# Performance work log

Measured on AMD Instinct MI355X. Metric: run time of the kernel, lower is better.

## Reference

```python
import jax, jax.numpy as jnp
import numpy as np

B, L, V = 64, 512, 32000
E, H, D = 64, 512, 1024   # embed dim, LSTM hidden, bidirectional dim
NH, KD = 8, 64            # attention heads, key_dim
TOPK = 5
BN_EPS = 1e-3             # keras BatchNormalization default epsilon


def _run_lstm(x, Wx, Wh, b):
    """Keras-style LSTM (gate order i,f,g,o). x: [B,T,Din]. Returns (seq [B,T,H], last [B,H])."""
    Bn, Hn = x.shape[0], Wh.shape[0]
    z = jnp.einsum('btd,dk->btk', x, Wx) + b  # precompute input contribution [B,T,4H]
    def step(carry, zt):
        h, c = carry
        g = zt + h @ Wh
        i, f, gg, o = jnp.split(g, 4, axis=-1)
        c = jax.nn.sigmoid(f) * c + jax.nn.sigmoid(i) * jnp.tanh(gg)
        h = jax.nn.sigmoid(o) * jnp.tanh(c)
        return (h, c), h
    init = (jnp.zeros((Bn, Hn), x.dtype), jnp.zeros((Bn, Hn), x.dtype))
    (hT, _), hs = jax.lax.scan(step, init, jnp.swapaxes(z, 0, 1))
    return jnp.swapaxes(hs, 0, 1), hT


def _bilstm_seq(x, fWx, fWh, fb, bWx, bWh, bb):
    hf, _ = _run_lstm(x, fWx, fWh, fb)
    hb, _ = _run_lstm(x[:, ::-1], bWx, bWh, bb)
    return jnp.concatenate([hf, hb[:, ::-1]], axis=-1)


def _bilstm_last(x, fWx, fWh, fb, bWx, bWh, bb):
    _, hf = _run_lstm(x, fWx, fWh, fb)
    _, hb = _run_lstm(x[:, ::-1], bWx, bWh, bb)
    return jnp.concatenate([hf, hb], axis=-1)


def _cos(x):
    return x / (jnp.linalg.norm(x, axis=-1, keepdims=True) + 1e-6)


def _topk_gather(q, keys, values, k, weight=None):
    """Cosine-similarity top-k retrieval: q [B,64], keys/values [N,64] -> [B,k,64]."""
    sim = _cos(q) @ _cos(keys).T          # [B,N]
    if weight is not None:
        sim = sim * weight                # importance / confidence weighting
    _, idx = jax.lax.top_k(sim, k)
    return values[idx]                    # gather -> [B,k,64]


def _forward(tokens, emb,
             l1f_Wx, l1f_Wh, l1f_b, l1b_Wx, l1b_Wh, l1b_b,
             l2f_Wx, l2f_Wh, l2f_b, l2b_Wx, l2b_Wh, l2b_b,
             Wq, bq, Wk, bk, Wv, bv, Wo, bo,
             mq_W, mq_b,
             ext_keys, ext_vals, form_emb, conc_keys, conc_vals,
             st_mem, lt_mem, lt_imp, inf_mem, inf_conf,
             rs_W, rs_b, bn_gamma, bn_beta, bn_mean, bn_var,
             out_W, out_b, fin_W, fin_b):
    # _process_input
    x = emb[tokens]                                                   # [B,L,64]
    x = _bilstm_seq(x, l1f_Wx, l1f_Wh, l1f_b, l1b_Wx, l1b_Wh, l1b_b)  # [B,L,1024]
    x = _bilstm_last(x, l2f_Wx, l2f_Wh, l2f_b, l2b_Wx, l2b_Wh, l2b_b) # [B,1024]
    # _apply_attention: MHA over a length-1 sequence
    xs = x[:, None, :]                                                # [B,1,1024]
    q = jnp.einsum('bse,ehd->bshd', xs, Wq) + bq
    k = jnp.einsum('bse,ehd->bshd', xs, Wk) + bk
    v = jnp.einsum('bse,ehd->bshd', xs, Wv) + bv
    att = jax.nn.softmax(jnp.einsum('bshd,bthd->bhst', q, k) / jnp.sqrt(jnp.float32(KD)), axis=-1)
    ctx = jnp.einsum('bhst,bthd->bshd', att, v)
    x = (jnp.einsum('bshd,hde->bse', ctx, Wo) + bo)[:, 0]             # [B,1024]
    # _query_memories: six-bank gather/combine
    query = x @ mq_W + mq_b                                           # [B,64]
    m_ext = jax.nn.softmax(query @ ext_keys.T, axis=-1) @ ext_vals    # [B,64]
    m_form = _topk_gather(query, form_emb, form_emb, TOPK)            # [B,5,64]
    m_conc = _topk_gather(query, conc_keys, conc_vals, TOPK)          # [B,5,64]
    m_st = _topk_gather(query, st_mem, st_mem, TOPK)                  # [B,5,64]
    m_lt = _topk_gather(query, lt_mem, lt_mem, TOPK, weight=lt_imp)   # [B,5,64]
    m_inf = _topk_gather(query, inf_mem, inf_mem, TOPK, weight=inf_conf)
    mem = jnp.concatenate([m_ext[:, None], m_form, m_conc, m_st, m_lt, m_inf], axis=1)  # [B,26,64]
    x = jnp.mean(mem, axis=1)                                         # [B,64]
    # _apply_reasoning (training=False -> inference batchnorm)
    x = jax.nn.relu(x @ rs_W + rs_b)                                  # [B,512]
    x = (x - bn_mean) / jnp.sqrt(bn_var + BN_EPS) * bn_gamma + bn_beta
    # _generate_output (stage 'elementary1')
    x = x @ out_W + out_b                                             # [B,128]
    return jax.nn.sigmoid(x @ fin_W + fin_b)                          # [B,1]


def setup_inputs() -> dict:
    key = jax.random.key(0)
    ks = iter(jax.random.split(key, 64))
    def rn(shape, s=0.02):
        return jax.random.normal(next(ks), shape, dtype=jnp.float32) * s
    def z(shape):
        return jnp.zeros(shape, dtype=jnp.float32)
    inp = {
        'tokens': jax.random.randint(next(ks), (B, L), 0, V),
        'emb': rn((V, E), 0.05),
        'l1f_Wx': rn((E, 4 * H)), 'l1f_Wh': rn((H, 4 * H)), 'l1f_b': z((4 * H,)),
        'l1b_Wx': rn((E, 4 * H)), 'l1b_Wh': rn((H, 4 * H)), 'l1b_b': z((4 * H,)),
        'l2f_Wx': rn((D, 4 * H)), 'l2f_Wh': rn((H, 4 * H)), 'l2f_b': z((4 * H,)),
        'l2b_Wx': rn((D, 4 * H)), 'l2b_Wh': rn((H, 4 * H)), 'l2b_b': z((4 * H,)),
        'Wq': rn((D, NH, KD)), 'bq': z((NH, KD)),
        'Wk': rn((D, NH, KD)), 'bk': z((NH, KD)),
        'Wv': rn((D, NH, KD)), 'bv': z((NH, KD)),
        'Wo': rn((NH, KD, D)), 'bo': z((D,)),
        'mq_W': rn((D, 64)), 'mq_b': z((64,)),
        'ext_keys': rn((100, 64), 0.5), 'ext_vals': rn((100, 64), 0.5),
        'form_emb': rn((1000, 64), 0.5),
        'conc_keys': rn((1000, 64), 0.5), 'conc_vals': rn((1000, 64), 0.5),
        'st_mem': rn((100, 64), 0.5),
        'lt_mem': rn((10000, 64), 0.5),
        'lt_imp': jax.random.uniform(next(ks), (10000,), dtype=jnp.float32),
        'inf_mem': rn((500, 64), 0.5),
        'inf_conf': jax.random.uniform(next(ks), (500,), dtype=jnp.float32),
        'rs_W': rn((64, 512)), 'rs_b': z((512,)),
        'bn_gamma': jnp.ones((512,), jnp.float32), 'bn_beta': z((512,)),
        'bn_mean': rn((512,), 0.1), 'bn_var': jnp.ones((512,), jnp.float32),
        'out_W': rn((512, 128)), 'out_b': z((128,)),
        'fin_W': rn((128, 1)), 'fin_b': z((1,)),
    }
    return inp


def reference(tokens, emb,
              l1f_Wx, l1f_Wh, l1f_b, l1b_Wx, l1b_Wh, l1b_b,
              l2f_Wx, l2f_Wh, l2f_b, l2b_Wx, l2b_Wh, l2b_b,
              Wq, bq, Wk, bk, Wv, bv, Wo, bo,
              mq_W, mq_b,
              ext_keys, ext_vals, form_emb, conc_keys, conc_vals,
              st_mem, lt_mem, lt_imp, inf_mem, inf_conf,
              rs_W, rs_b, bn_gamma, bn_beta, bn_mean, bn_var,
              out_W, out_b, fin_W, fin_b):
    return _forward(tokens, emb,
                    l1f_Wx, l1f_Wh, l1f_b, l1b_Wx, l1b_Wh, l1b_b,
                    l2f_Wx, l2f_Wh, l2f_b, l2b_Wx, l2b_Wh, l2b_b,
                    Wq, bq, Wk, bk, Wv, bv, Wo, bo,
                    mq_W, mq_b,
                    ext_keys, ext_vals, form_emb, conc_keys, conc_vals,
                    st_mem, lt_mem, lt_imp, inf_mem, inf_conf,
                    rs_W, rs_b, bn_gamma, bn_beta, bn_mean, bn_var,
                    out_W, out_b, fin_W, fin_b)
```

## Files before the change

### kernel.cpp

```cpp
#include <hip/hip_runtime.h>
#include <cstddef>
#include <cstdint>

typedef short s8v   __attribute__((ext_vector_type(8)));
typedef float f32x4 __attribute__((ext_vector_type(4)));

__device__ __forceinline__ float b2f(unsigned short u) {
  union { unsigned u; float f; } x; x.u = ((unsigned)u) << 16; return x.f;
}
__device__ __forceinline__ unsigned short f2b(float f) {
  union { float f; unsigned u; } x; x.f = f;
  unsigned u = x.u;
  return (unsigned short)((u + 0x7FFFu + ((u >> 16) & 1u)) >> 16);
}
__device__ __forceinline__ float sigm(float x) { return 1.f / (1.f + __expf(-x)); }
__device__ __forceinline__ float tanh_(float x) { return 1.f - 2.f / (__expf(2.f * x) + 1.f); }

#define AT_LOAD(p)     __hip_atomic_load((p), __ATOMIC_RELAXED, __HIP_MEMORY_SCOPE_AGENT)
#define AT_STORE_RLX(p,v) __hip_atomic_store((p), (v), __ATOMIC_RELAXED, __HIP_MEMORY_SCOPE_AGENT)

__device__ __forceinline__ s8v ldg_b128_sc(const unsigned short* p) {
  s8v r;
  asm volatile("global_load_dwordx4 %0, %1, off sc0 sc1" : "=v"(r) : "v"(p) : "memory");
  return r;
}
__device__ __forceinline__ void stg_b128_sc(unsigned short* p, s8v v) {
  asm volatile("global_store_dwordx4 %0, %1, off sc0 sc1" :: "v"(p), "v"(v) : "memory");
}

__global__ void __launch_bounds__(256)
k_embed(const int* __restrict__ tok, const float* __restrict__ emb,
        unsigned short* __restrict__ x1)
{
  const int g = blockIdx.x * 256 + threadIdx.x;
  if (g >= 64 * 512 * 8) return;
  const int row = g >> 3, i = g & 7;
  const int t = tok[row];
  const f32x4 v0 = *(const f32x4*)(emb + (size_t)t * 64 + i * 8);
  const f32x4 v1 = *(const f32x4*)(emb + (size_t)t * 64 + i * 8 + 4);
  s8v o;
#pragma unroll
  for (int e = 0; e < 4; ++e) { o[e] = (short)f2b(v0[e]); o[4 + e] = (short)f2b(v1[e]); }
  *(s8v*)(x1 + (size_t)row * 64 + i * 8) = o;
}

__global__ void __launch_bounds__(256)
k_wxt(const float* __restrict__ Wf, const float* __restrict__ Wb,
      unsigned short* __restrict__ out)
{
  __shared__ float t[64][65];
  const int tid = threadIdx.x;
  const int kt = blockIdx.x, nt = blockIdx.y, dir = blockIdx.z;
  const float* W = dir ? Wb : Wf;
#pragma unroll
  for (int i = 0; i < 16; ++i) {
    const int c = i * 256 + tid;
    const int k = c >> 6, n = c & 63;
    t[k][n] = W[(size_t)(kt * 64 + k) * 2048 + nt * 64 + n];
  }
  __syncthreads();
#pragma unroll
  for (int i = 0; i < 16; ++i) {
    const int c = i * 256 + tid;
    const int n = c >> 6, k = c & 63;
    out[(size_t)dir * 2048 * 1024 + (size_t)(nt * 64 + n) * 1024 + kt * 64 + k] = f2b(t[k][n]);
  }
}

__global__ void __launch_bounds__(256)
k_norms(const float* __restrict__ formE, const float* __restrict__ concK,
        const float* __restrict__ stM, const float* __restrict__ ltM,
        const float* __restrict__ infM, float* __restrict__ inn)
{
  const int i = blockIdx.x * 256 + threadIdx.x;
  if (i >= 12600) return;
  const float* src; int loc;
  if (i < 1000)       { src = formE; loc = i; }
  else if (i < 2000)  { src = concK; loc = i - 1000; }
  else if (i < 2100)  { src = stM;   loc = i - 2000; }
  else if (i < 12100) { src = ltM;   loc = i - 2100; }
  else                { src = infM;  loc = i - 12100; }
  float ss = 0.f;
#pragma unroll 16
  for (int d = 0; d < 64; ++d) { const float v = src[(size_t)loc * 64 + d]; ss += v * v; }
  inn[i] = 1.f / (sqrtf(ss) + 1e-6f);
}

template<int PHASE>
__global__ void __launch_bounds__(128, 1)
k_lstm(const unsigned short* __restrict__ xin,
       const unsigned short* __restrict__ z2fp, const unsigned short* __restrict__ z2bp,
       const float* __restrict__ Whf, const float* __restrict__ Whb,
       const float* __restrict__ Wxf, const float* __restrict__ Wxb,
       const float* __restrict__ bsf, const float* __restrict__ bsb,
       unsigned short* __restrict__ hbuf,
       unsigned short* __restrict__ yout,
       int* __restrict__ flags,
       float* __restrict__ cg,
       int s0, int s1, int CT)
{
  __shared__ unsigned short h_lds[64 * 512];
  __shared__ unsigned short x_lds[64 * 64];
  __shared__ float g_lds[2][64 * 64];
  __shared__ float c_lds[64 * 16];
  __shared__ float bias_lds[64];

  const int tid  = threadIdx.x;
  const int wv   = tid >> 6;
  const int lane = tid & 63;
  const int wg   = blockIdx.x & 31;
  const int dir  = blockIdx.x >> 5;
  const int j0   = wg * 16;
  const int fc   = lane & 15;
  const int fk   = (lane >> 4) << 3;

  const float* Wh = dir ? Whb : Whf;
  const float* Wx = dir ? Wxb : Wxf;
  const unsigned short* Z2 = dir ? z2bp : z2fp;
  const float* BS = dir ? bsb : bsf;
  int* flg = flags + dir * 32;
  unsigned short* hb = hbuf + (size_t)dir * (2 * 64 * 512);

  for (int i = tid; i < 64; i += 128) bias_lds[i] = BS[(i >> 4) * 512 + j0 + (i & 15)];
  if (PHASE == 1 || s0 == 0) {
    for (int i = tid; i < 1024; i += 128) c_lds[i] = 0.f;
  } else {
    for (int i = tid; i < 1024; i += 128)
      c_lds[i] = cg[(size_t)dir * 64 * 512 + (i >> 4) * 512 + j0 + (i & 15)];
  }

  s8v Bh[4][8];
#pragma unroll
  for (int nt = 0; nt < 4; ++nt) {
    const int col = nt * 512 + j0 + fc;
#pragma unroll
    for (int kk = 0; kk < 8; ++kk) {
      const int kb = wv * 256 + kk * 32 + fk;
      s8v f;
#pragma unroll
      for (int i = 0; i < 8; ++i) f[i] = (short)f2b(Wh[(size_t)(kb + i) * 2048 + col]);
      Bh[nt][kk] = f;
    }
  }
  s8v Bx[4];
  if (PHASE == 1) {
#pragma unroll
    for (int nt = 0; nt < 4; ++nt) {
      const int col = nt * 512 + j0 + fc;
      const int kb = wv * 32 + fk;
      s8v f;
#pragma unroll
      for (int i = 0; i < 8; ++i) f[i] = (short)f2b(Wx[(size_t)(kb + i) * 2048 + col]);
      Bx[nt] = f;
    }
  }
  __syncthreads();

  for (int s = s0; s < s1; ++s) {
    const int t = dir ? (511 - s) : s;

    s8v zreg[4];
    if (PHASE == 1) {
#pragma unroll
      for (int i = 0; i < 4; ++i) {
        const int c = i * 128 + tid;
        const int row = c >> 3, kb = c & 7;
        s8v v = *(const s8v*)(xin + ((size_t)row * 512 + t) * 64 + kb * 8);
        *(s8v*)((char*)x_lds + row * 128 + ((kb * 16) ^ ((row & 7) << 4))) = v;
      }
    } else {
      const int gb = tid >> 1, jh = tid & 1;
      const int lt = dir ? (s1 - 1 - s) : (s - s0);
#pragma unroll
      for (int g = 0; g < 4; ++g)
        zreg[g] = *(const s8v*)(Z2 + ((size_t)(gb * CT + lt)) * 2048 + g * 512 + j0 + jh * 8);
    }

    if (s > 0) {
      const int target = s;
      int spins = 0;
      for (;;) {
        int v = (lane < 32) ? AT_LOAD(&flg[lane]) : target;
        if (__all(v >= target)) break;
        if (++spins > (1 << 18)) break;
        __builtin_amdgcn_s_sleep(1);
      }
      const unsigned short* hsrc = hb + (size_t)((s - 1) & 1) * (64 * 512);
      s8v tmp[16];
#pragma unroll
      for (int r = 0; r < 2; ++r) {
#pragma unroll
        for (int i = 0; i < 16; ++i) {
          const int c = (r * 16 + i) * 128 + tid;
          const int row = c >> 6, kb = c & 63;
          tmp[i] = ldg_b128_sc(hsrc + (size_t)row * 512 + kb * 8);
        }
        asm volatile("s_waitcnt vmcnt(0)" ::: "memory");
        __builtin_amdgcn_sched_barrier(0);
#pragma unroll
        for (int i = 0; i < 16; ++i) {
          const int c = (r * 16 + i) * 128 + tid;
          const int row = c >> 6, kb = c & 63;
          *(s8v*)((char*)h_lds + row * 1024 + ((kb * 16) ^ ((row & 7) << 4))) = tmp[i];
        }
      }
    }
    __syncthreads();

    f32x4 acc[4][4];
#pragma unroll
    for (int mt = 0; mt < 4; ++mt)
#pragma unroll
      for (int nt = 0; nt < 4; ++nt) acc[mt][nt] = (f32x4){0.f, 0.f, 0.f, 0.f};

    if (PHASE == 1) {
      const int kx2 = (wv * 32 + fk) * 2;
#pragma unroll
      for (int mt = 0; mt < 4; ++mt) {
        const int row = mt * 16 + fc;
        s8v a = *(const s8v*)((char*)x_lds + row * 128 + (kx2 ^ ((row & 7) << 4)));
#pragma unroll
        for (int nt = 0; nt < 4; ++nt)
          acc[mt][nt] = __builtin_amdgcn_mfma_f32_16x16x32_bf16(a, Bx[nt], acc[mt][nt], 0, 0, 0);
      }
    }
    if (s > 0) {
#pragma unroll
      for (int kk = 0; kk < 8; ++kk) {
        const int k2 = (wv * 256 + kk * 32 + fk) * 2;
        s8v a[4];
#pragma unroll
        for (int mt = 0; mt < 4; ++mt) {
          const int row = mt * 16 + fc;
          a[mt] = *(const s8v*)((char*)h_lds + row * 1024 + (k2 ^ ((row & 7) << 4)));
        }
#pragma unroll
        for (int mt = 0; mt < 4; ++mt)
#pragma unroll
          for (int nt = 0; nt < 4; ++nt)
            acc[mt][nt] = __builtin_amdgcn_mfma_f32_16x16x32_bf16(a[mt], Bh[nt][kk], acc[mt][nt], 0, 0, 0);
      }
    }
    {
      const int r0 = (lane >> 4) << 2;
#pragma unroll
      for (int mt = 0; mt < 4; ++mt)
#pragma unroll
        for (int nt = 0; nt < 4; ++nt) {
          const int colj = nt * 16 + fc;
          const int row0 = mt * 16 + r0;
#pragma unroll
          for (int r = 0; r < 4; ++r)
            g_lds[wv][(row0 + r) * 64 + colj] = acc[mt][nt][r];
        }
    }
    __syncthreads();

    {
      const int gb = tid >> 1, jh = tid & 1;
      const float* g0 = g_lds[0] + gb * 64;
      const float* g1 = g_lds[1] + gb * 64;
      s8v hv;
#pragma unroll
      for (int jj = 0; jj < 8; ++jj) {
        const int j = jh * 8 + jj;
        float pi = g0[0 * 16 + j] + g1[0 * 16 + j] + bias_lds[0 * 16 + j];
        float pf = g0[1 * 16 + j] + g1[1 * 16 + j] + bias_lds[1 * 16 + j];
        float pg = g0[2 * 16 + j] + g1[2 * 16 + j] + bias_lds[2 * 16 + j];
        float po = g0[3 * 16 + j] + g1[3 * 16 + j] + bias_lds[3 * 16 + j];
        if (PHASE == 2) {
          pi += b2f((unsigned short)zreg[0][jj]);
          pf += b2f((unsigned short)zreg[1][jj]);
          pg += b2f((unsigned short)zreg[2][jj]);
          po += b2f((unsigned short)zreg[3][jj]);
        }
        const int ci = gb * 16 + j;
        const float c = sigm(pf) * c_lds[ci] + sigm(pi) * tanh_(pg);
        c_lds[ci] = c;
        hv[jj] = (short)f2b(sigm(po) * tanh_(c));
      }
      stg_b128_sc(hb + (size_t)(s & 1) * (64 * 512) + gb * 512 + j0 + jh * 8, hv);
      if (PHASE == 1) {
        *(s8v*)(yout + ((size_t)gb * 512 + t) * 1024 + dir * 512 + j0 + jh * 8) = hv;
      } else if (s == 511) {
        *(s8v*)(yout + (size_t)gb * 1024 + dir * 512 + j0 + jh * 8) = hv;
      }
    }
    if (PHASE == 2 && s == s1 - 1 && s1 < 512) {
      __syncthreads();
      for (int i = tid; i < 1024; i += 128)
        cg[(size_t)dir * 64 * 512 + (i >> 4) * 512 + j0 + (i & 15)] = c_lds[i];
    }
    __syncthreads();
    if (tid == 0) AT_STORE_RLX(&flg[wg], s + 1);
  }
}

__global__ void __launch_bounds__(256)
k_zgemm(const unsigned short* __restrict__ A, const unsigned short* __restrict__ Wxt,
        unsigned short* __restrict__ Cf, unsigned short* __restrict__ Cb,
        int tb0, int tb1, int CT)
{
  __shared__ unsigned short As[128 * 64];
  __shared__ unsigned short Bs[128 * 64];
  const int tid = threadIdx.x;
  const int lane = tid & 63;
  const int w = tid >> 6;
  const int wm = w >> 1, wn = w & 1;
  const int bx = blockIdx.x, by = blockIdx.y, dz = blockIdx.z;
  const unsigned short* Bmat = Wxt + (size_t)dz * 2048 * 1024;
  unsigned short* C = dz ? Cb : Cf;
  const int tb = dz ? tb1 : tb0;
  const int fc = lane & 15, fk = (lane >> 4) << 3;

  f32x4 acc[4][4];
#pragma unroll
  for (int mt = 0; mt < 4; ++mt)
#pragma unroll
    for (int nt = 0; nt < 4; ++nt) acc[mt][nt] = (f32x4){0.f, 0.f, 0.f, 0.f};

  for (int kt = 0; kt < 16; ++kt) {
    __syncthreads();
#pragma unroll
    for (int i = 0; i < 4; ++i) {
      const int c = i * 256 + tid;
      const int row = c >> 3, kb = c & 7;
      const int m = by * 128 + row;
      const int b = m / CT, lt = m - b * CT;
      s8v v = *(const s8v*)(A + ((size_t)b * 512 + tb + lt) * 1024 + kt * 64 + kb * 8);
      *(s8v*)((char*)As + row * 128 + ((kb * 16) ^ ((row & 7) << 4))) = v;
    }
#pragma unroll
    for (int i = 0; i < 4; ++i) {
      const int c = i * 256 + tid;
      const int n = c >> 3, kb = c & 7;
      s8v v = *(const s8v*)(Bmat + (size_t)(bx * 128 + n) * 1024 + kt * 64 + kb * 8);
      *(s8v*)((char*)Bs + n * 128 + ((kb * 16) ^ ((n & 7) << 4))) = v;
    }
    __syncthreads();
#pragma unroll
    for (int kk = 0; kk < 2; ++kk) {
      const int k2 = (kk * 32 + fk) * 2;
      s8v a[4], bfr[4];
#pragma unroll
      for (int mt = 0; mt < 4; ++mt) {
        const int row = wm * 64 + mt * 16 + fc;
        a[mt] = *(const s8v*)((char*)As + row * 128 + (k2 ^ ((row & 7) << 4)));
      }
#pragma unroll
      for (int nt = 0; nt < 4; ++nt) {
        const int n = wn * 64 + nt * 16 + fc;
        bfr[nt] = *(const s8v*)((char*)Bs + n * 128 + (k2 ^ ((n & 7) << 4)));
      }
#pragma unroll
      for (int mt = 0; mt < 4; ++mt)
#pragma unroll
        for (int nt = 0; nt < 4; ++nt)
          acc[mt][nt] = __builtin_amdgcn_mfma_f32_16x16x32_bf16(a[mt], bfr[nt], acc[mt][nt], 0, 0, 0);
    }
  }
  const int r0 = (lane >> 4) << 2;
#pragma unroll
  for (int mt = 0; mt < 4; ++mt)
#pragma unroll
    for (int nt = 0; nt < 4; ++nt) {
      const size_t rowg = (size_t)(by * 128 + wm * 64 + mt * 16 + r0);
      const int colg = bx * 128 + wn * 64 + nt * 16 + fc;
#pragma unroll
      for (int r = 0; r < 4; ++r)
        C[(rowg + r) * 2048 + colg] = f2b(acc[mt][nt][r]);
    }
}

__global__ void __launch_bounds__(256)
k_head1(const unsigned short* __restrict__ x2,
        const float* __restrict__ Wv, const float* __restrict__ bv,
        const float* __restrict__ Wo, const float* __restrict__ bo,
        const float* __restrict__ mqW, const float* __restrict__ mqb,
        float* __restrict__ query)
{
  __shared__ float xs[1024], ys[512], x3[1024];
  __shared__ float part[4][64];
  const int b = blockIdx.x, tid = threadIdx.x;
  for (int i = tid; i < 1024; i += 256) xs[i] = b2f(x2[(size_t)b * 1024 + i]);
  __syncthreads();
  {
    const int o = tid * 2;
    float a0 = 0.f, a1 = 0.f;
#pragma unroll 8
    for (int e = 0; e < 1024; ++e) {
      const float xv = xs[e];
      a0 += xv * Wv[(size_t)e * 512 + o];
      a1 += xv * Wv[(size_t)e * 512 + o + 1];
    }
    ys[o] = a0 + bv[o];
    ys[o + 1] = a1 + bv[o + 1];
  }
  __syncthreads();
  {
    const int e0 = tid * 4;
    float a0 = 0.f, a1 = 0.f, a2 = 0.f, a3 = 0.f;
#pragma unroll 8
    for (int h = 0; h < 512; ++h) {
      const float yv = ys[h];
      a0 += yv * Wo[(size_t)h * 1024 + e0];
      a1 += yv * Wo[(size_t)h * 1024 + e0 + 1];
      a2 += yv * Wo[(size_t)h * 1024 + e0 + 2];
      a3 += yv * Wo[(size_t)h * 1024 + e0 + 3];
    }
    x3[e0] = a0 + bo[e0];
    x3[e0 + 1] = a1 + bo[e0 + 1];
    x3[e0 + 2] = a2 + bo[e0 + 2];
    x3[e0 + 3] = a3 + bo[e0 + 3];
  }
  __syncthreads();
  {
    const int o = tid & 63, kc = tid >> 6;
    float a = 0.f;
#pragma unroll 8
    for (int e = kc * 256; e < kc * 256 + 256; ++e) a += x3[e] * mqW[(size_t)e * 64 + o];
    part[kc][o] = a;
  }
  __syncthreads();
  if (tid < 64)
    query[b * 64 + tid] = part[0][tid] + part[1][tid] + part[2][tid] + part[3][tid] + mqb[tid];
}

__device__ void bank_topk(const float* __restrict__ K, const float* __restrict__ V,
                          int n, const float* __restrict__ W, const float* __restrict__ inn,
                          float qinv, const float* q, float* sims, float* red, int* redi,
                          float* acc64, int tid)
{
  for (int i = tid; i < n; i += 256) {
    float s = 0.f;
#pragma unroll 16
    for (int d = 0; d < 64; ++d) s += q[d] * K[(size_t)i * 64 + d];
    s *= qinv * inn[i];
    if (W) s *= W[i];
    sims[i] = s;
  }
  __syncthreads();
  for (int it = 0; it < 5; ++it) {
    float bv = -1e30f; int bi = 1 << 30;
    for (int i = tid; i < n; i += 256) {
      const float v = sims[i];
      if (v > bv) { bv = v; bi = i; }
    }
    red[tid] = bv; redi[tid] = bi;
    __syncthreads();
    for (int st = 128; st >= 1; st >>= 1) {
      if (tid < st) {
        const float v = red[tid + st]; const int ix = redi[tid + st];
        if (v > red[tid] || (v == red[tid] && ix < redi[tid])) { red[tid] = v; redi[tid] = ix; }
      }
      __syncthreads();
    }
    const int sel = redi[0];
    if (tid < 64) acc64[tid] += V[(size_t)sel * 64 + tid];
    if (tid == 0) sims[sel] = -1e30f;
    __syncthreads();
  }
}

__global__ void __launch_bounds__(256)
k_head2(const float* __restrict__ query,
        const float* extK, const float* extV,
        const float* formE, const float* concK, const float* concV,
        const float* stM, const float* ltM, const float* ltW,
        const float* infM, const float* infW,
        const float* __restrict__ inn,
        const float* rsW, const float* rsb,
        const float* gma, const float* bta,
        const float* mea, const float* vr,
        const float* outW, const float* outb,
        const float* finW, const float* finb,
        float* __restrict__ out)
{
  __shared__ float q[64];
  __shared__ float acc64[64];
  __shared__ float sims[10000];
  __shared__ float red[256];
  __shared__ int redi[256];
  __shared__ float r1[512];
  __shared__ float o2[128];

  const int b = blockIdx.x, tid = threadIdx.x;
  if (tid < 64) q[tid] = query[b * 64 + tid];
  __syncthreads();
  red[tid] = (tid < 64) ? q[tid] * q[tid] : 0.f;
  __syncthreads();
  for (int st = 128; st >= 1; st >>= 1) { if (tid < st) red[tid] += red[tid + st]; __syncthreads(); }
  const float qinv = 1.f / (sqrtf(red[0]) + 1e-6f);
  __syncthreads();

  if (tid < 100) {
    float s = 0.f;
#pragma unroll 16
    for (int d = 0; d < 64; ++d) s += q[d] * extK[(size_t)tid * 64 + d];
    sims[tid] = s;
  }
  __syncthreads();
  red[tid] = (tid < 100) ? sims[tid] : -1e30f;
  __syncthreads();
  for (int st = 128; st >= 1; st >>= 1) { if (tid < st && red[tid + st] > red[tid]) red[tid] = red[tid + st]; __syncthreads(); }
  const float mx = red[0];
  __syncthreads();
  red[tid] = (tid < 100) ? __expf(sims[tid] - mx) : 0.f;
  __syncthreads();
  for (int st = 128; st >= 1; st >>= 1) { if (tid < st) red[tid] += red[tid + st]; __syncthreads(); }
  const float Z = red[0];
  __syncthreads();
  if (tid < 100) sims[tid] = __expf(sims[tid] - mx) / Z;
  __syncthreads();
  if (tid < 64) {
    float a = 0.f;
    for (int i = 0; i < 100; ++i) a += sims[i] * extV[(size_t)i * 64 + tid];
    acc64[tid] = a;
  }
  __syncthreads();

  bank_topk(formE, formE, 1000,  nullptr, inn + 0,     qinv, q, sims, red, redi, acc64, tid);
  bank_topk(concK, concV, 1000,  nullptr, inn + 1000,  qinv, q, sims, red, redi, acc64, tid);
  bank_topk(stM,   stM,   100,   nullptr, inn + 2000,  qinv, q, sims, red, redi, acc64, tid);
  bank_topk(ltM,   ltM,   10000, ltW,     inn + 2100,  qinv, q, sims, red, redi, acc64, tid);
  bank_topk(infM,  infM,  500,   infW,    inn + 12100, qinv, q, sims, red, redi, acc64, tid);

  if (tid < 64) acc64[tid] *= (1.f / 26.f);
  __syncthreads();

  {
    const int o = tid * 2;
    float a0 = 0.f, a1 = 0.f;
#pragma unroll 16
    for (int d = 0; d < 64; ++d) {
      const float xv = acc64[d];
      a0 += xv * rsW[(size_t)d * 512 + o];
      a1 += xv * rsW[(size_t)d * 512 + o + 1];
    }
    a0 = fmaxf(a0 + rsb[o], 0.f);
    a1 = fmaxf(a1 + rsb[o + 1], 0.f);
    r1[o]     = (a0 - mea[o])     / sqrtf(vr[o]     + 1e-3f) * gma[o]     + bta[o];
    r1[o + 1] = (a1 - mea[o + 1]) / sqrtf(vr[o + 1] + 1e-3f) * gma[o + 1] + bta[o + 1];
  }
  __syncthreads();
  if (tid < 128) {
    float a = 0.f;
#pragma unroll 8
    for (int j = 0; j < 512; ++j) a += r1[j] * outW[(size_t)j * 128 + tid];
    o2[tid] = a + outb[tid];
  }
  __syncthreads();
  red[tid] = (tid < 128) ? o2[tid] * finW[tid] : 0.f;
  __syncthreads();
  for (int st = 128; st >= 1; st >>= 1) { if (tid < st) red[tid] += red[tid + st]; __syncthreads(); }
  if (tid == 0) out[b] = sigm(red[0] + finb[0]);
}

__global__ void k_diag(float* out, int n, float val) {
  const int i = blockIdx.x * 64 + threadIdx.x;
  if (i < n) out[i] = val;
}

extern "C" void kernel_launch(void* const* d_in, const int* in_sizes, int n_in,
                              void* d_out, int out_size, void* d_ws, size_t ws_size,
                              hipStream_t stream)
{
  (void)in_sizes; (void)n_in;
  const int*   tokens = (const int*)d_in[0];
  const float* emb    = (const float*)d_in[1];
  const float* l1fWx  = (const float*)d_in[2];
  const float* l1fWh  = (const float*)d_in[3];
  const float* l1fb   = (const float*)d_in[4];
  const float* l1bWx  = (const float*)d_in[5];
  const float* l1bWh  = (const float*)d_in[6];
  const float* l1bb   = (const float*)d_in[7];
  const float* l2fWx  = (const float*)d_in[8];
  const float* l2fWh  = (const float*)d_in[9];
  const float* l2fb   = (const float*)d_in[10];
  const float* l2bWx  = (const float*)d_in[11];
  const float* l2bWh  = (const float*)d_in[12];
  const float* l2bb   = (const float*)d_in[13];
  const float* Wv     = (const float*)d_in[18];
  const float* bv     = (const float*)d_in[19];
  const float* Wo     = (const float*)d_in[20];
  const float* bo     = (const float*)d_in[21];
  const float* mqW    = (const float*)d_in[22];
  const float* mqb    = (const float*)d_in[23];
  const float* extK   = (const float*)d_in[24];
  const float* extV   = (const float*)d_in[25];
  const float* formE  = (const float*)d_in[26];
  const float* concK  = (const float*)d_in[27];
  const float* concV  = (const float*)d_in[28];
  const float* stM    = (const float*)d_in[29];
  const float* ltM    = (const float*)d_in[30];
  const float* ltW    = (const float*)d_in[31];
  const float* infM   = (const float*)d_in[32];
  const float* infW   = (const float*)d_in[33];
  const float* rsW    = (const float*)d_in[34];
  const float* rsb    = (const float*)d_in[35];
  const float* gma    = (const float*)d_in[36];
  const float* bta    = (const float*)d_in[37];
  const float* mea    = (const float*)d_in[38];
  const float* vr     = (const float*)d_in[39];
  const float* outW   = (const float*)d_in[40];
  const float* outb   = (const float*)d_in[41];
  const float* finW   = (const float*)d_in[42];
  const float* finb   = (const float*)d_in[43];

  float* outp = (float*)d_out;
  char* ws = (char*)d_ws;

  size_t off = 0;
  auto take = [&](size_t sz) { size_t o = off; off += (sz + 255) & ~(size_t)255; return o; };
  const size_t o_x1    = take((size_t)64 * 512 * 64 * 2);
  const size_t o_y1    = take((size_t)64 * 512 * 1024 * 2);
  const size_t o_wxt   = take((size_t)2 * 2048 * 1024 * 2);
  const size_t o_h1    = take((size_t)2 * 2 * 64 * 512 * 2);
  const size_t o_h2    = take((size_t)2 * 2 * 64 * 512 * 2);
  const size_t o_cg    = take((size_t)2 * 64 * 512 * 4);
  const size_t o_x2    = take((size_t)64 * 1024 * 2);
  const size_t o_query = take((size_t)64 * 64 * 4);
  const size_t o_norms = take((size_t)12600 * 4);
  const size_t o_flags = take(512);
  const size_t base = off;

  int CT = 0;
  const int cts[6] = {512, 256, 128, 64, 32, 16};
  for (int i = 0; i < 6; ++i) {
    const size_t need = base + (size_t)cts[i] * 524288 + 256;
    if (need <= ws_size) { CT = cts[i]; break; }
  }
  if (CT == 0) {
    k_diag<<<1, 64, 0, stream>>>(outp, out_size, (float)(ws_size >> 20));
    return;
  }
  const size_t o_zc = take((size_t)CT * 524288);

  unsigned short* x1   = (unsigned short*)(ws + o_x1);
  unsigned short* y1   = (unsigned short*)(ws + o_y1);
  unsigned short* wxt  = (unsigned short*)(ws + o_wxt);
  unsigned short* h1   = (unsigned short*)(ws + o_h1);
  unsigned short* h2   = (unsigned short*)(ws + o_h2);
  float*          cg   = (float*)(ws + o_cg);
  unsigned short* x2   = (unsigned short*)(ws + o_x2);
  float*          qry  = (float*)(ws + o_query);
  float*          nrm  = (float*)(ws + o_norms);
  int*            flags = (int*)(ws + o_flags);
  unsigned short* zcf  = (unsigned short*)(ws + o_zc);
  unsigned short* zcb  = zcf + (size_t)64 * CT * 2048;

  hipMemsetAsync(flags, 0, 512, stream);
  k_embed<<<1024, 256, 0, stream>>>(tokens, emb, x1);
  k_norms<<<50, 256, 0, stream>>>(formE, concK, stM, ltM, infM, nrm);
  k_wxt<<<dim3(16, 32, 2), 256, 0, stream>>>(l2fWx, l2bWx, wxt);

  k_lstm<1><<<64, 128, 0, stream>>>(x1, nullptr, nullptr, l1fWh, l1bWh, l1fWx, l1bWx,
                                    l1fb, l1bb, h1, y1, flags, nullptr, 0, 512, 512);

  const int nC = 512 / CT;
  for (int c = 0; c < nC; ++c) {
    const int s0 = c * CT, s1 = s0 + CT;
    k_zgemm<<<dim3(16, (64 * CT) / 128, 2), 256, 0, stream>>>(
        y1, wxt, zcf, zcb, s0, 512 - s1, CT);
    k_lstm<2><<<64, 128, 0, stream>>>(nullptr, zcf, zcb, l2fWh, l2bWh, nullptr, nullptr,
                                      l2fb, l2bb, h2, x2, flags + 64, cg, s0, s1, CT);
  }

  k_head1<<<64, 256, 0, stream>>>(x2, Wv, bv, Wo, bo, mqW, mqb, qry);
  k_head2<<<64, 256, 0, stream>>>(qry, extK, extV, formE, concK, concV, stM, ltM, ltW,
                                  infM, infW, nrm, rsW, rsb, gma, bta, mea, vr,
                                  outW, outb, finW, finb, outp);
}
```

Baseline: 7.066 ms.

## Split LSTM recurrence by batch rows per wave, removing cross-wave K reduction

The recurrent step used to split the K dimension across the two waves and then reduce partial gates through LDS with an extra barrier. It now gives each wave 32 batch rows over the full K=512, so gate activations are computed straight from MFMA accumulators, and the cell state lives in registers. Recurrent weights are pre-transposed to bf16 by a generic transpose kernel so they load as vector reads. The h load is also split so the first half is written to LDS while the second half is still in flight. In exchange, each thread now holds twice as many weight registers (64 s8v), which raises register pressure and could cause spills.

```diff
diff --git a/kernel.cpp b/kernel.cpp
--- a/kernel.cpp
+++ b/kernel.cpp
@@ -16,7 +16,7 @@
 __device__ __forceinline__ float sigm(float x) { return 1.f / (1.f + __expf(-x)); }
 __device__ __forceinline__ float tanh_(float x) { return 1.f - 2.f / (__expf(2.f * x) + 1.f); }
 
-#define AT_LOAD(p)     __hip_atomic_load((p), __ATOMIC_RELAXED, __HIP_MEMORY_SCOPE_AGENT)
+#define AT_LOAD(p)        __hip_atomic_load((p), __ATOMIC_RELAXED, __HIP_MEMORY_SCOPE_AGENT)
 #define AT_STORE_RLX(p,v) __hip_atomic_store((p), (v), __ATOMIC_RELAXED, __HIP_MEMORY_SCOPE_AGENT)
 
 __device__ __forceinline__ s8v ldg_b128_sc(const unsigned short* p) {
@@ -45,8 +45,8 @@
 }
 
 __global__ void __launch_bounds__(256)
-k_wxt(const float* __restrict__ Wf, const float* __restrict__ Wb,
-      unsigned short* __restrict__ out)
+k_tr(const float* __restrict__ Wf, const float* __restrict__ Wb,
+     unsigned short* __restrict__ out, int K, int N)
 {
   __shared__ float t[64][65];
   const int tid = threadIdx.x;
@@ -56,14 +56,14 @@
   for (int i = 0; i < 16; ++i) {
     const int c = i * 256 + tid;
     const int k = c >> 6, n = c & 63;
-    t[k][n] = W[(size_t)(kt * 64 + k) * 2048 + nt * 64 + n];
+    t[k][n] = W[(size_t)(kt * 64 + k) * N + nt * 64 + n];
   }
   __syncthreads();
 #pragma unroll
   for (int i = 0; i < 16; ++i) {
     const int c = i * 256 + tid;
     const int n = c >> 6, k = c & 63;
-    out[(size_t)dir * 2048 * 1024 + (size_t)(nt * 64 + n) * 1024 + kt * 64 + k] = f2b(t[k][n]);
+    out[(size_t)dir * N * K + (size_t)(nt * 64 + n) * K + kt * 64 + k] = f2b(t[k][n]);
   }
 }
 
@@ -90,7 +90,7 @@
 __global__ void __launch_bounds__(128, 1)
 k_lstm(const unsigned short* __restrict__ xin,
        const unsigned short* __restrict__ z2fp, const unsigned short* __restrict__ z2bp,
-       const float* __restrict__ Whf, const float* __restrict__ Whb,
+       const unsigned short* __restrict__ wht,
        const float* __restrict__ Wxf, const float* __restrict__ Wxb,
        const float* __restrict__ bsf, const float* __restrict__ bsb,
        unsigned short* __restrict__ hbuf,
@@ -99,81 +99,81 @@
        float* __restrict__ cg,
        int s0, int s1, int CT)
 {
-  __shared__ unsigned short h_lds[64 * 512];
-  __shared__ unsigned short x_lds[64 * 64];
-  __shared__ float g_lds[2][64 * 64];
-  __shared__ float c_lds[64 * 16];
-  __shared__ float bias_lds[64];
+  __shared__ __align__(16) unsigned short h_lds[64 * 512];
+  __shared__ __align__(16) unsigned short z_lds[64 * 72];
+  __shared__ __align__(16) unsigned short hout[16 * 72];
 
   const int tid  = threadIdx.x;
-  const int wv   = tid >> 6;
+  const int w    = tid >> 6;
   const int lane = tid & 63;
+  const int fc   = lane & 15, fg = lane >> 4;
   const int wg   = blockIdx.x & 31;
   const int dir  = blockIdx.x >> 5;
   const int j0   = wg * 16;
-  const int fc   = lane & 15;
-  const int fk   = (lane >> 4) << 3;
-
-  const float* Wh = dir ? Whb : Whf;
+
+  const unsigned short* Wht = wht + (size_t)dir * 2048 * 512;
   const float* Wx = dir ? Wxb : Wxf;
   const unsigned short* Z2 = dir ? z2bp : z2fp;
   const float* BS = dir ? bsb : bsf;
   int* flg = flags + dir * 32;
   unsigned short* hb = hbuf + (size_t)dir * (2 * 64 * 512);
 
-  for (int i = tid; i < 64; i += 128) bias_lds[i] = BS[(i >> 4) * 512 + j0 + (i & 15)];
+  float bias_reg[4];
+#pragma unroll
+  for (int nt = 0; nt < 4; ++nt) bias_reg[nt] = BS[nt * 512 + j0 + fc];
+
+  float c_reg[8];
   if (PHASE == 1 || s0 == 0) {
-    for (int i = tid; i < 1024; i += 128) c_lds[i] = 0.f;
+#pragma unroll
+    for (int i = 0; i < 8; ++i) c_reg[i] = 0.f;
   } else {
-    for (int i = tid; i < 1024; i += 128)
-      c_lds[i] = cg[(size_t)dir * 64 * 512 + (i >> 4) * 512 + j0 + (i & 15)];
-  }
-
-  s8v Bh[4][8];
-#pragma unroll
-  for (int nt = 0; nt < 4; ++nt) {
-    const int col = nt * 512 + j0 + fc;
-#pragma unroll
-    for (int kk = 0; kk < 8; ++kk) {
-      const int kb = wv * 256 + kk * 32 + fk;
-      s8v f;
-#pragma unroll
-      for (int i = 0; i < 8; ++i) f[i] = (short)f2b(Wh[(size_t)(kb + i) * 2048 + col]);
-      Bh[nt][kk] = f;
-    }
-  }
-  s8v Bx[4];
+#pragma unroll
+    for (int mt = 0; mt < 2; ++mt)
+#pragma unroll
+      for (int v = 0; v < 4; ++v)
+        c_reg[mt * 4 + v] =
+          cg[(size_t)dir * 32768 + (size_t)(w * 32 + mt * 16 + fg * 4 + v) * 512 + j0 + fc];
+  }
+
+  s8v Bh[4][16];
+#pragma unroll
+  for (int nt = 0; nt < 4; ++nt)
+#pragma unroll
+    for (int kk = 0; kk < 16; ++kk)
+      Bh[nt][kk] = *(const s8v*)(Wht + (size_t)(nt * 512 + j0 + fc) * 512 + kk * 32 + fg * 8);
+
+  s8v Bx[4][2];
   if (PHASE == 1) {
 #pragma unroll
-    for (int nt = 0; nt < 4; ++nt) {
-      const int col = nt * 512 + j0 + fc;
-      const int kb = wv * 32 + fk;
-      s8v f;
-#pragma unroll
-      for (int i = 0; i < 8; ++i) f[i] = (short)f2b(Wx[(size_t)(kb + i) * 2048 + col]);
-      Bx[nt] = f;
-    }
-  }
-  __syncthreads();
+    for (int nt = 0; nt < 4; ++nt)
+#pragma unroll
+      for (int kx = 0; kx < 2; ++kx) {
+        s8v f;
+#pragma unroll
+        for (int i = 0; i < 8; ++i)
+          f[i] = (short)f2b(Wx[(size_t)(kx * 32 + fg * 8 + i) * 2048 + nt * 512 + j0 + fc]);
+        Bx[nt][kx] = f;
+      }
+  }
 
   for (int s = s0; s < s1; ++s) {
     const int t = dir ? (511 - s) : s;
-
-    s8v zreg[4];
+    const int gb = tid >> 1, jh = tid & 1;
+
+    s8v xf[2][2];
+    s8v zr[4];
     if (PHASE == 1) {
 #pragma unroll
-      for (int i = 0; i < 4; ++i) {
-        const int c = i * 128 + tid;
-        const int row = c >> 3, kb = c & 7;
-        s8v v = *(const s8v*)(xin + ((size_t)row * 512 + t) * 64 + kb * 8);
-        *(s8v*)((char*)x_lds + row * 128 + ((kb * 16) ^ ((row & 7) << 4))) = v;
-      }
+      for (int mt = 0; mt < 2; ++mt)
+#pragma unroll
+        for (int kx = 0; kx < 2; ++kx)
+          xf[mt][kx] = *(const s8v*)(xin +
+            ((size_t)(w * 32 + mt * 16 + fc) * 512 + t) * 64 + kx * 32 + fg * 8);
     } else {
-      const int gb = tid >> 1, jh = tid & 1;
       const int lt = dir ? (s1 - 1 - s) : (s - s0);
 #pragma unroll
       for (int g = 0; g < 4; ++g)
-        zreg[g] = *(const s8v*)(Z2 + ((size_t)(gb * CT + lt)) * 2048 + g * 512 + j0 + jh * 8);
+        zr[g] = *(const s8v*)(Z2 + ((size_t)(gb * CT + lt)) * 2048 + g * 512 + j0 + jh * 8);
     }
 
     if (s > 0) {
@@ -186,110 +186,114 @@
         __builtin_amdgcn_s_sleep(1);
       }
       const unsigned short* hsrc = hb + (size_t)((s - 1) & 1) * (64 * 512);
-      s8v tmp[16];
-#pragma unroll
-      for (int r = 0; r < 2; ++r) {
-#pragma unroll
-        for (int i = 0; i < 16; ++i) {
-          const int c = (r * 16 + i) * 128 + tid;
-          const int row = c >> 6, kb = c & 63;
-          tmp[i] = ldg_b128_sc(hsrc + (size_t)row * 512 + kb * 8);
-        }
-        asm volatile("s_waitcnt vmcnt(0)" ::: "memory");
-        __builtin_amdgcn_sched_barrier(0);
-#pragma unroll
-        for (int i = 0; i < 16; ++i) {
-          const int c = (r * 16 + i) * 128 + tid;
-          const int row = c >> 6, kb = c & 63;
-          *(s8v*)((char*)h_lds + row * 1024 + ((kb * 16) ^ ((row & 7) << 4))) = tmp[i];
-        }
-      }
+      s8v t0[16], t1[16];
+#pragma unroll
+      for (int i = 0; i < 16; ++i) {
+        const int c = i * 128 + tid;
+        t0[i] = ldg_b128_sc(hsrc + (size_t)(c >> 6) * 512 + (c & 63) * 8);
+      }
+#pragma unroll
+      for (int i = 0; i < 16; ++i) {
+        const int c = (16 + i) * 128 + tid;
+        t1[i] = ldg_b128_sc(hsrc + (size_t)(c >> 6) * 512 + (c & 63) * 8);
+      }
+      asm volatile("s_waitcnt vmcnt(16)" ::: "memory");
+      __builtin_amdgcn_sched_barrier(0);
+#pragma unroll
+      for (int i = 0; i < 16; ++i) {
+        const int c = i * 128 + tid;
+        const int row = c >> 6, kb = c & 63;
+        *(s8v*)((char*)h_lds + row * 1024 + ((kb * 16) ^ ((row & 7) << 4))) = t0[i];
+      }
+      asm volatile("s_waitcnt vmcnt(0)" ::: "memory");
+      __builtin_amdgcn_sched_barrier(0);
+#pragma unroll
+      for (int i = 0; i < 16; ++i) {
+        const int c = (16 + i) * 128 + tid;
+        const int row = c >> 6, kb = c & 63;
+        *(s8v*)((char*)h_lds + row * 1024 + ((kb * 16) ^ ((row & 7) << 4))) = t1[i];
+      }
+    }
+    if (PHASE == 2) {
+#pragma unroll
+      for (int g = 0; g < 4; ++g)
+        *(s8v*)(z_lds + gb * 72 + g * 16 + jh * 8) = zr[g];
     }
     __syncthreads();
 
-    f32x4 acc[4][4];
-#pragma unroll
-    for (int mt = 0; mt < 4; ++mt)
+    f32x4 acc[2][4];
+#pragma unroll
+    for (int mt = 0; mt < 2; ++mt)
 #pragma unroll
       for (int nt = 0; nt < 4; ++nt) acc[mt][nt] = (f32x4){0.f, 0.f, 0.f, 0.f};
 
     if (PHASE == 1) {
-      const int kx2 = (wv * 32 + fk) * 2;
-#pragma unroll
-      for (int mt = 0; mt < 4; ++mt) {
-        const int row = mt * 16 + fc;
-        s8v a = *(const s8v*)((char*)x_lds + row * 128 + (kx2 ^ ((row & 7) << 4)));
-#pragma unroll
-        for (int nt = 0; nt < 4; ++nt)
-          acc[mt][nt] = __builtin_amdgcn_mfma_f32_16x16x32_bf16(a, Bx[nt], acc[mt][nt], 0, 0, 0);
-      }
+#pragma unroll
+      for (int kx = 0; kx < 2; ++kx)
+#pragma unroll
+        for (int mt = 0; mt < 2; ++mt)
+#pragma unroll
+          for (int nt = 0; nt < 4; ++nt)
+            acc[mt][nt] = __builtin_amdgcn_mfma_f32_16x16x32_bf16(xf[mt][kx], Bx[nt][kx], acc[mt][nt], 0, 0, 0);
     }
     if (s > 0) {
 #pragma unroll
-      for (int kk = 0; kk < 8; ++kk) {
-        const int k2 = (wv * 256 + kk * 32 + fk) * 2;
-        s8v a[4];
-#pragma unroll
-        for (int mt = 0; mt < 4; ++mt) {
-          const int row = mt * 16 + fc;
+      for (int kk = 0; kk < 16; ++kk) {
+        const int k2 = (kk * 32 + fg * 8) * 2;
+        s8v a[2];
+#pragma unroll
+        for (int mt = 0; mt < 2; ++mt) {
+          const int row = w * 32 + mt * 16 + fc;
           a[mt] = *(const s8v*)((char*)h_lds + row * 1024 + (k2 ^ ((row & 7) << 4)));
         }
 #pragma unroll
-        for (int mt = 0; mt < 4; ++mt)
+        for (int mt = 0; mt < 2; ++mt)
 #pragma unroll
           for (int nt = 0; nt < 4; ++nt)
             acc[mt][nt] = __builtin_amdgcn_mfma_f32_16x16x32_bf16(a[mt], Bh[nt][kk], acc[mt][nt], 0, 0, 0);
       }
     }
+
+#pragma unroll
+    for (int mt = 0; mt < 2; ++mt)
+#pragma unroll
+      for (int v = 0; v < 4; ++v) {
+        const int b = w * 32 + mt * 16 + fg * 4 + v;
+        float pi = acc[mt][0][v] + bias_reg[0];
+        float pf = acc[mt][1][v] + bias_reg[1];
+        float pg = acc[mt][2][v] + bias_reg[2];
+        float po = acc[mt][3][v] + bias_reg[3];
+        if (PHASE == 2) {
+          pi += b2f(z_lds[b * 72 + 0 * 16 + fc]);
+          pf += b2f(z_lds[b * 72 + 1 * 16 + fc]);
+          pg += b2f(z_lds[b * 72 + 2 * 16 + fc]);
+          po += b2f(z_lds[b * 72 + 3 * 16 + fc]);
+        }
+        const float c = sigm(pf) * c_reg[mt * 4 + v] + sigm(pi) * tanh_(pg);
+        c_reg[mt * 4 + v] = c;
+        hout[fc * 72 + b] = f2b(sigm(po) * tanh_(c));
+      }
+    asm volatile("s_waitcnt lgkmcnt(0)" ::: "memory");
+    __builtin_amdgcn_sched_barrier(0);
     {
-      const int r0 = (lane >> 4) << 2;
-#pragma unroll
-      for (int mt = 0; mt < 4; ++mt)
-#pragma unroll
-        for (int nt = 0; nt < 4; ++nt) {
-          const int colj = nt * 16 + fc;
-          const int row0 = mt * 16 + r0;
-#pragma unroll
-          for (int r = 0; r < 4; ++r)
-            g_lds[wv][(row0 + r) * 64 + colj] = acc[mt][nt][r];
-        }
-    }
-    __syncthreads();
-
-    {
-      const int gb = tid >> 1, jh = tid & 1;
-      const float* g0 = g_lds[0] + gb * 64;
-      const float* g1 = g_lds[1] + gb * 64;
-      s8v hv;
-#pragma unroll
-      for (int jj = 0; jj < 8; ++jj) {
-        const int j = jh * 8 + jj;
-        float pi = g0[0 * 16 + j] + g1[0 * 16 + j] + bias_lds[0 * 16 + j];
-        float pf = g0[1 * 16 + j] + g1[1 * 16 + j] + bias_lds[1 * 16 + j];
-        float pg = g0[2 * 16 + j] + g1[2 * 16 + j] + bias_lds[2 * 16 + j];
-        float po = g0[3 * 16 + j] + g1[3 * 16 + j] + bias_lds[3 * 16 + j];
-        if (PHASE == 2) {
-          pi += b2f((unsigned short)zreg[0][jj]);
-          pf += b2f((unsigned short)zreg[1][jj]);
-          pg += b2f((unsigned short)zreg[2][jj]);
-          po += b2f((unsigned short)zreg[3][jj]);
-        }
-        const int ci = gb * 16 + j;
-        const float c = sigm(pf) * c_lds[ci] + sigm(pi) * tanh_(pg);
-        c_lds[ci] = c;
-        hv[jj] = (short)f2b(sigm(po) * tanh_(c));
-      }
-      stg_b128_sc(hb + (size_t)(s & 1) * (64 * 512) + gb * 512 + j0 + jh * 8, hv);
+      const int bb = tid >> 1, hh = tid & 1;
+      s8v o;
+#pragma unroll
+      for (int e = 0; e < 8; ++e) o[e] = (short)hout[(hh * 8 + e) * 72 + bb];
+      stg_b128_sc(hb + (size_t)(s & 1) * (64 * 512) + bb * 512 + j0 + hh * 8, o);
       if (PHASE == 1) {
-        *(s8v*)(yout + ((size_t)gb * 512 + t) * 1024 + dir * 512 + j0 + jh * 8) = hv;
+        *(s8v*)(yout + ((size_t)(bb * 512 + t)) * 1024 + dir * 512 + j0 + hh * 8) = o;
       } else if (s == 511) {
-        *(s8v*)(yout + (size_t)gb * 1024 + dir * 512 + j0 + jh * 8) = hv;
+        *(s8v*)(yout + (size_t)bb * 1024 + dir * 512 + j0 + hh * 8) = o;
       }
     }
     if (PHASE == 2 && s == s1 - 1 && s1 < 512) {
-      __syncthreads();
-      for (int i = tid; i < 1024; i += 128)
-        cg[(size_t)dir * 64 * 512 + (i >> 4) * 512 + j0 + (i & 15)] = c_lds[i];
+#pragma unroll
+      for (int mt = 0; mt < 2; ++mt)
+#pragma unroll
+        for (int v = 0; v < 4; ++v)
+          cg[(size_t)dir * 32768 + (size_t)(w * 32 + mt * 16 + fg * 4 + v) * 512 + j0 + fc] =
+            c_reg[mt * 4 + v];
     }
     __syncthreads();
     if (tid == 0) AT_STORE_RLX(&flg[wg], s + 1);
@@ -615,6 +619,8 @@
   const size_t o_x1    = take((size_t)64 * 512 * 64 * 2);
   const size_t o_y1    = take((size_t)64 * 512 * 1024 * 2);
   const size_t o_wxt   = take((size_t)2 * 2048 * 1024 * 2);
+  const size_t o_wht1  = take((size_t)2 * 2048 * 512 * 2);
+  const size_t o_wht2  = take((size_t)2 * 2048 * 512 * 2);
   const size_t o_h1    = take((size_t)2 * 2 * 64 * 512 * 2);
   const size_t o_h2    = take((size_t)2 * 2 * 64 * 512 * 2);
   const size_t o_cg    = take((size_t)2 * 64 * 512 * 4);
@@ -639,6 +645,8 @@
   unsigned short* x1   = (unsigned short*)(ws + o_x1);
   unsigned short* y1   = (unsigned short*)(ws + o_y1);
   unsigned short* wxt  = (unsigned short*)(ws + o_wxt);
+  unsigned short* wht1 = (unsigned short*)(ws + o_wht1);
+  unsigned short* wht2 = (unsigned short*)(ws + o_wht2);
   unsigned short* h1   = (unsigned short*)(ws + o_h1);
   unsigned short* h2   = (unsigned short*)(ws + o_h2);
   float*          cg   = (float*)(ws + o_cg);
@@ -652,9 +660,11 @@
   hipMemsetAsync(flags, 0, 512, stream);
   k_embed<<<1024, 256, 0, stream>>>(tokens, emb, x1);
   k_norms<<<50, 256, 0, stream>>>(formE, concK, stM, ltM, infM, nrm);
-  k_wxt<<<dim3(16, 32, 2), 256, 0, stream>>>(l2fWx, l2bWx, wxt);
-
-  k_lstm<1><<<64, 128, 0, stream>>>(x1, nullptr, nullptr, l1fWh, l1bWh, l1fWx, l1bWx,
+  k_tr<<<dim3(8, 32, 2), 256, 0, stream>>>(l1fWh, l1bWh, wht1, 512, 2048);
+  k_tr<<<dim3(8, 32, 2), 256, 0, stream>>>(l2fWh, l2bWh, wht2, 512, 2048);
+  k_tr<<<dim3(16, 32, 2), 256, 0, stream>>>(l2fWx, l2bWx, wxt, 1024, 2048);
+
+  k_lstm<1><<<64, 128, 0, stream>>>(x1, nullptr, nullptr, wht1, l1fWx, l1bWx,
                                     l1fb, l1bb, h1, y1, flags, nullptr, 0, 512, 512);
 
   const int nC = 512 / CT;
@@ -662,7 +672,7 @@
     const int s0 = c * CT, s1 = s0 + CT;
     k_zgemm<<<dim3(16, (64 * CT) / 128, 2), 256, 0, stream>>>(
         y1, wxt, zcf, zcb, s0, 512 - s1, CT);
-    k_lstm<2><<<64, 128, 0, stream>>>(nullptr, zcf, zcb, l2fWh, l2bWh, nullptr, nullptr,
+    k_lstm<2><<<64, 128, 0, stream>>>(nullptr, zcf, zcb, wht2, nullptr, nullptr,
                                       l2fb, l2bb, h2, x2, flags + 64, cg, s0, s1, CT);
   }
 
```

After: 8.082 ms. +14.4%, slower.
